# Performance work log

Hardware: AMD Instinct MI355X
Metric: run time of the kernel (lower is better)

The kernel has to match this reference:

```python
import jax, jax.numpy as jnp
import numpy as np

B, S, D, H, A = 2, 2048, 1024, 16, 64
INIT_STD = 0.02


def setup_inputs() -> dict:
    key = jax.random.key(0)
    ks = jax.random.split(key, 5)
    return {
        "residual": jax.random.normal(ks[0], (B, S, D), dtype=jnp.float32),
        "Wq": jax.random.normal(ks[1], (H, D, A), dtype=jnp.float32) * INIT_STD,
        "Wk": jax.random.normal(ks[2], (H, D, A), dtype=jnp.float32) * INIT_STD,
        "Wv": jax.random.normal(ks[3], (H, D, A), dtype=jnp.float32) * INIT_STD,
        "Wo": jax.random.normal(ks[4], (H, A, D), dtype=jnp.float32) * INIT_STD,
        "bq": jnp.zeros((H, A), dtype=jnp.float32),
        "bk": jnp.zeros((H, A), dtype=jnp.float32),
        "bv": jnp.zeros((H, A), dtype=jnp.float32),
        "bo": jnp.zeros((D,), dtype=jnp.float32),
    }


def reference(residual, Wq, Wk, Wv, Wo, bq, bk, bv, bo):
    # residual: [B,S,D]; W{q,k,v}: [H,D,A]; Wo: [H,A,D]
    q = jnp.einsum("bsd,hda->bhsa", residual, Wq) + bq[None, :, None, :]
    k = jnp.einsum("bsd,hda->bhsa", residual, Wk) + bk[None, :, None, :]
    v = jnp.einsum("bsd,hda->bhsa", residual, Wv) + bv[None, :, None, :]
    scale = 1.0 / jnp.sqrt(jnp.float32(q.shape[-1]))
    scores = jnp.einsum("bhsa,bhta->bhst", q, k) * scale  # [B,H,S,S]
    s = scores.shape[-1]
    causal = jnp.tril(jnp.ones((s, s), dtype=bool))  # True = keep
    # original masked_fill with -100000.0 (not -inf); stay faithful
    masked = jnp.where(causal, scores, jnp.float32(-100000.0))
    pattern = jax.nn.softmax(masked, axis=-1)
    z = jnp.einsum("bhst,bhta->bshа".replace("а", "a"), pattern, v)  # [B,S,H,A]
    out = jnp.einsum("bsha,had->bsd", z, Wo) + bo
    return out
```

## Files before the change

kernel.cpp:

```cpp
#include <hip/hip_runtime.h>
#include <hip/hip_bf16.h>

#define B_ 2
#define S_ 2048
#define D_ 1024
#define H_ 16
#define A_ 64

typedef __attribute__((ext_vector_type(8))) short bf16x8;
typedef __attribute__((ext_vector_type(4))) float f32x4;

#define QSCALE 0.1803368801111204f

__device__ inline short f2bf(float f) {
    union { float f; unsigned u; } x; x.f = f;
    unsigned r = x.u + 0x7fff + ((x.u >> 16) & 1);
    return (short)(r >> 16);
}

__device__ inline float dpp_max16(float x) {
    int v;
    v = __builtin_amdgcn_update_dpp(0, __builtin_bit_cast(int, x), 0xB1, 0xF, 0xF, false);
    x = fmaxf(x, __builtin_bit_cast(float, v));
    v = __builtin_amdgcn_update_dpp(0, __builtin_bit_cast(int, x), 0x4E, 0xF, 0xF, false);
    x = fmaxf(x, __builtin_bit_cast(float, v));
    v = __builtin_amdgcn_update_dpp(0, __builtin_bit_cast(int, x), 0x141, 0xF, 0xF, false);
    x = fmaxf(x, __builtin_bit_cast(float, v));
    v = __builtin_amdgcn_update_dpp(0, __builtin_bit_cast(int, x), 0x140, 0xF, 0xF, false);
    x = fmaxf(x, __builtin_bit_cast(float, v));
    return x;
}
__device__ inline float dpp_sum16(float x) {
    int v;
    v = __builtin_amdgcn_update_dpp(0, __builtin_bit_cast(int, x), 0xB1, 0xF, 0xF, false);
    x += __builtin_bit_cast(float, v);
    v = __builtin_amdgcn_update_dpp(0, __builtin_bit_cast(int, x), 0x4E, 0xF, 0xF, false);
    x += __builtin_bit_cast(float, v);
    v = __builtin_amdgcn_update_dpp(0, __builtin_bit_cast(int, x), 0x141, 0xF, 0xF, false);
    x += __builtin_bit_cast(float, v);
    v = __builtin_amdgcn_update_dpp(0, __builtin_bit_cast(int, x), 0x140, 0xF, 0xF, false);
    x += __builtin_bit_cast(float, v);
    return x;
}

__global__ __launch_bounds__(256) void cast_kernel(const float* __restrict__ x,
                                                   short* __restrict__ y, int n) {
    int i = (blockIdx.x * 256 + threadIdx.x) * 8;
    if (i < n) {
        float4 a = *(const float4*)(x + i);
        float4 b = *(const float4*)(x + i + 4);
        bf16x8 o;
        o[0]=f2bf(a.x); o[1]=f2bf(a.y); o[2]=f2bf(a.z); o[3]=f2bf(a.w);
        o[4]=f2bf(b.x); o[5]=f2bf(b.y); o[6]=f2bf(b.z); o[7]=f2bf(b.w);
        *(bf16x8*)(y + i) = o;
    }
}

__global__ __launch_bounds__(256) void wtrans_kernel(
    const float* __restrict__ Wq, const float* __restrict__ Wk,
    const float* __restrict__ Wv, const float* __restrict__ Wo,
    short* __restrict__ Wt, short* __restrict__ Wot) {
    const int kt = blockIdx.x, yy = blockIdx.y, z = blockIdx.z;
    __shared__ short T[64 * 72];
    const int tid = threadIdx.x;
    const int r = tid >> 2, c0 = (tid & 3) * 16;
    const float* src;
    if (z < 3) {
        const float* W = z == 0 ? Wq : (z == 1 ? Wk : Wv);
        src = &W[yy * (D_ * A_) + (kt * 64 + r) * A_ + c0];
    } else {
        src = &Wo[(kt * 64 + r) * D_ + yy * 64 + c0];
    }
    #pragma unroll
    for (int q = 0; q < 4; q++) {
        float4 f = *(const float4*)(src + q * 4);
        T[r * 72 + c0 + q * 4 + 0] = f2bf(f.x);
        T[r * 72 + c0 + q * 4 + 1] = f2bf(f.y);
        T[r * 72 + c0 + q * 4 + 2] = f2bf(f.z);
        T[r * 72 + c0 + q * 4 + 3] = f2bf(f.w);
    }
    __syncthreads();
    const int a = tid >> 2, kc = (tid & 3) * 16;
    bf16x8 o0, o1;
    #pragma unroll
    for (int j = 0; j < 8; j++) {
        o0[j] = T[(kc + j) * 72 + a];
        o1[j] = T[(kc + 8 + j) * 72 + a];
    }
    const int n_base = (z < 3) ? z * 1024 + yy * 64 : yy * 64;
    short* dst = (z < 3) ? &Wt[(n_base + a) * D_ + kt * 64 + kc]
                         : &Wot[(n_base + a) * D_ + kt * 64 + kc];
    *(bf16x8*)dst = o0;
    *(bf16x8*)(dst + 8) = o1;
}

__global__ __launch_bounds__(256) void qkv_gemm(
    const short* __restrict__ X, const short* __restrict__ Wt,
    const float* __restrict__ bq, const float* __restrict__ bk, const float* __restrict__ bv,
    short* __restrict__ Qb, short* __restrict__ Kb, short* __restrict__ Vt) {
    const int mt = blockIdx.x, nt = blockIdx.y;
    const int m0 = mt * 128, n0 = nt * 128;
    const int sel = n0 >> 10;
    __shared__ short Xl[2][128 * 40], Wl[2][128 * 40];
    const int tid = threadIdx.x, wv = tid >> 6, lane = tid & 63, quad = lane >> 4, l16 = lane & 15;
    const int grow = tid >> 1, gk = (tid & 1) * 16;
    f32x4 acc[4][4] = {};
    bf16x8 xr0, xr1, wr0, wr1;
    {
        const short* xs = &X[(m0 + grow) * D_ + gk];
        xr0 = *(const bf16x8*)xs; xr1 = *(const bf16x8*)(xs + 8);
        const short* wsp = &Wt[(n0 + grow) * D_ + gk];
        wr0 = *(const bf16x8*)wsp; wr1 = *(const bf16x8*)(wsp + 8);
    }
    const int rm = (wv & 1) * 64, cn = (wv >> 1) * 64;
    for (int i = 0; i < 32; i++) {
        const int bu = i & 1;
        *(bf16x8*)&Xl[bu][grow * 40 + gk]     = xr0;
        *(bf16x8*)&Xl[bu][grow * 40 + gk + 8] = xr1;
        *(bf16x8*)&Wl[bu][grow * 40 + gk]     = wr0;
        *(bf16x8*)&Wl[bu][grow * 40 + gk + 8] = wr1;
        __syncthreads();
        if (i < 31) {
            const int k0 = (i + 1) * 32;
            const short* xs = &X[(m0 + grow) * D_ + k0 + gk];
            xr0 = *(const bf16x8*)xs; xr1 = *(const bf16x8*)(xs + 8);
            const short* wsp = &Wt[(n0 + grow) * D_ + k0 + gk];
            wr0 = *(const bf16x8*)wsp; wr1 = *(const bf16x8*)(wsp + 8);
        }
        bf16x8 af[4];
        #pragma unroll
        for (int rt = 0; rt < 4; rt++)
            af[rt] = *(bf16x8*)&Xl[bu][(rm + rt * 16 + l16) * 40 + quad * 8];
        #pragma unroll
        for (int ct = 0; ct < 4; ct++) {
            bf16x8 bf = *(bf16x8*)&Wl[bu][(cn + ct * 16 + l16) * 40 + quad * 8];
            #pragma unroll
            for (int rt = 0; rt < 4; rt++)
                acc[rt][ct] = __builtin_amdgcn_mfma_f32_16x16x32_bf16(af[rt], bf, acc[rt][ct], 0, 0, 0);
        }
    }
    const int b = m0 >> 11;
    const float* bias = sel == 0 ? bq : (sel == 1 ? bk : bv);
    if (sel < 2) {
        short* dst = sel == 0 ? Qb : Kb;
        const float scale = sel == 0 ? QSCALE : 1.0f;
        #pragma unroll
        for (int ct = 0; ct < 4; ct++) {
            const int n = n0 + cn + ct * 16 + l16;
            const int h = (n >> 6) & 15, a = n & 63;
            const float bi = bias[n & 1023];
            #pragma unroll
            for (int rt = 0; rt < 4; rt++)
                #pragma unroll
                for (int r = 0; r < 4; r++) {
                    const int row = m0 + rm + rt * 16 + quad * 4 + r;
                    const int s = row & (S_ - 1);
                    dst[(((b * H_) + h) * S_ + s) * A_ + a] = f2bf((acc[rt][ct][r] + bi) * scale);
                }
        }
    } else {
        #pragma unroll
        for (int ct = 0; ct < 4; ct++) {
            const int n = n0 + cn + ct * 16 + l16;
            const int h = (n >> 6) & 15, a = n & 63;
            const float bi = bias[n & 1023];
            #pragma unroll
            for (int rt = 0; rt < 4; rt++) {
                short4 pk;
                pk.x = f2bf(acc[rt][ct][0] + bi);
                pk.y = f2bf(acc[rt][ct][1] + bi);
                pk.z = f2bf(acc[rt][ct][2] + bi);
                pk.w = f2bf(acc[rt][ct][3] + bi);
                const int row = m0 + rm + rt * 16 + quad * 4;
                const int s = row & (S_ - 1);
                *(short4*)&Vt[(((b * H_) + h) * A_ + a) * S_ + s] = pk;
            }
        }
    }
}

__global__ __launch_bounds__(512, 4) void flash_kernel(
    const short* __restrict__ Qb, const short* __restrict__ Kb,
    const short* __restrict__ Vt, short* __restrict__ Z) {
    const int p = blockIdx.x, h = blockIdx.y, b = blockIdx.z;
    const int bh = b * H_ + h;
    const int qlo = p, qhi = 31 - p;
    __shared__ short Kl[2][4096], Vl[2][4096];
    __shared__ short Pl[8][1024];
    const int tid = threadIdx.x, wv = tid >> 6, lane = tid & 63, quad = lane >> 4, l16 = lane & 15;
    const int wg = wv & 3;
    const int myqt = (wv < 4) ? qhi : qlo;
    short* Pw = &Pl[wv][0];
    const int pbase = (l16 >> 3) * 128 + quad * 32 + (l16 & 7);

    const int L = tid;
    const int srow = (L >> 7) * 16 + (L & 15);
    const int scol = ((L >> 6) & 1) * 32 + ((L >> 4) & 3) * 8;

    const short* qptr = &Qb[(bh * S_ + myqt * 64 + wg * 16 + l16) * A_ + quad * 8];
    bf16x8 qf[2] = { *(const bf16x8*)qptr, *(const bf16x8*)(qptr + 32) };

    f32x4 O[4] = {};
    float m_i[4], l_i[4];
    #pragma unroll
    for (int r = 0; r < 4; r++) { m_i[r] = -1e30f; l_i[r] = 0.f; }

    bf16x8 kreg = *(const bf16x8*)&Kb[(bh * S_ + srow) * A_ + scol];
    bf16x8 vreg = *(const bf16x8*)&Vt[(bh * A_ + srow) * S_ + scol];

    for (int kt = 0; kt <= qhi; kt++) {
        const int bu = kt & 1;
        *(bf16x8*)&Kl[bu][L * 8] = kreg;
        *(bf16x8*)&Vl[bu][L * 8] = vreg;
        __syncthreads();
        if (kt < qhi) {
            kreg = *(const bf16x8*)&Kb[(bh * S_ + (kt + 1) * 64 + srow) * A_ + scol];
            vreg = *(const bf16x8*)&Vt[(bh * A_ + srow) * S_ + (kt + 1) * 64 + scol];
        }
        if (kt <= myqt) {
            f32x4 sacc[4] = {};
            #pragma unroll
            for (int kk = 0; kk < 2; kk++)
                #pragma unroll
                for (int ct = 0; ct < 4; ct++) {
                    bf16x8 kf = *(bf16x8*)&Kl[bu][((ct * 2 + kk) * 64 + lane) * 8];
                    sacc[ct] = __builtin_amdgcn_mfma_f32_16x16x32_bf16(qf[kk], kf, sacc[ct], 0, 0, 0);
                }
            if (kt == myqt) {
                #pragma unroll
                for (int ct = 0; ct < 4; ct++) {
                    const int cl = ct * 16 + l16;
                    #pragma unroll
                    for (int r = 0; r < 4; r++)
                        if (cl > wg * 16 + quad * 4 + r) sacc[ct][r] = -1e30f;
                }
            }
            #pragma unroll
            for (int r = 0; r < 4; r++) {
                float v = fmaxf(fmaxf(sacc[0][r], sacc[1][r]), fmaxf(sacc[2][r], sacc[3][r]));
                v = dpp_max16(v);
                const float mn = fmaxf(m_i[r], v);
                const float alpha = exp2f(m_i[r] - mn);
                float rs = 0.f;
                #pragma unroll
                for (int ct = 0; ct < 4; ct++) {
                    const float pe = exp2f(sacc[ct][r] - mn);
                    sacc[ct][r] = pe; rs += pe;
                }
                l_i[r] = l_i[r] * alpha + rs;
                m_i[r] = mn;
                #pragma unroll
                for (int ct = 0; ct < 4; ct++) O[ct][r] *= alpha;
            }
            #pragma unroll
            for (int ct = 0; ct < 4; ct++) {
                const int cb = pbase + (ct >> 1) * 512 + (ct & 1) * 256;
                #pragma unroll
                for (int r = 0; r < 4; r++)
                    Pw[cb + r * 8] = f2bf(sacc[ct][r]);
            }
            __builtin_amdgcn_s_waitcnt(0xC07F);
            bf16x8 pa0 = *(bf16x8*)&Pw[lane * 8];
            bf16x8 pa1 = *(bf16x8*)&Pw[(64 + lane) * 8];
            #pragma unroll
            for (int kk = 0; kk < 2; kk++)
                #pragma unroll
                for (int ct = 0; ct < 4; ct++) {
                    bf16x8 vf = *(bf16x8*)&Vl[bu][((ct * 2 + kk) * 64 + lane) * 8];
                    O[ct] = __builtin_amdgcn_mfma_f32_16x16x32_bf16(kk ? pa1 : pa0, vf, O[ct], 0, 0, 0);
                }
        }
    }
    float lsum[4];
    #pragma unroll
    for (int r = 0; r < 4; r++) lsum[r] = dpp_sum16(l_i[r]);
    #pragma unroll
    for (int ct = 0; ct < 4; ct++) {
        const int a = ct * 16 + l16;
        #pragma unroll
        for (int r = 0; r < 4; r++) {
            const int s = myqt * 64 + wg * 16 + quad * 4 + r;
            Z[(b * S_ + s) * (H_ * A_) + h * A_ + a] = f2bf(O[ct][r] / lsum[r]);
        }
    }
}

__global__ __launch_bounds__(256) void proj_gemm(
    const short* __restrict__ Zb, const short* __restrict__ Wot,
    const float* __restrict__ bo, float* __restrict__ out) {
    const int mt = blockIdx.x, nt = blockIdx.y;
    const int m0 = mt * 128, n0 = nt * 64;
    __shared__ short Xl[2][128 * 40], Wl[2][64 * 40];
    const int tid = threadIdx.x, wv = tid >> 6, lane = tid & 63, quad = lane >> 4, l16 = lane & 15;
    const int grow = tid >> 1, gk = (tid & 1) * 16;
    const bool doW = (tid < 128);
    f32x4 acc[4][2] = {};
    bf16x8 xr0, xr1, wr0, wr1;
    {
        const short* xs = &Zb[(m0 + grow) * D_ + gk];
        xr0 = *(const bf16x8*)xs; xr1 = *(const bf16x8*)(xs + 8);
        if (doW) {
            const short* wsp = &Wot[(n0 + grow) * D_ + gk];
            wr0 = *(const bf16x8*)wsp; wr1 = *(const bf16x8*)(wsp + 8);
        }
    }
    const int rm = (wv & 1) * 64, cn = (wv >> 1) * 32;
    for (int i = 0; i < 32; i++) {
        const int bu = i & 1;
        *(bf16x8*)&Xl[bu][grow * 40 + gk]     = xr0;
        *(bf16x8*)&Xl[bu][grow * 40 + gk + 8] = xr1;
        if (doW) {
            *(bf16x8*)&Wl[bu][grow * 40 + gk]     = wr0;
            *(bf16x8*)&Wl[bu][grow * 40 + gk + 8] = wr1;
        }
        __syncthreads();
        if (i < 31) {
            const int k0 = (i + 1) * 32;
            const short* xs = &Zb[(m0 + grow) * D_ + k0 + gk];
            xr0 = *(const bf16x8*)xs; xr1 = *(const bf16x8*)(xs + 8);
            if (doW) {
                const short* wsp = &Wot[(n0 + grow) * D_ + k0 + gk];
                wr0 = *(const bf16x8*)wsp; wr1 = *(const bf16x8*)(wsp + 8);
            }
        }
        bf16x8 af[4];
        #pragma unroll
        for (int rt = 0; rt < 4; rt++)
            af[rt] = *(bf16x8*)&Xl[bu][(rm + rt * 16 + l16) * 40 + quad * 8];
        #pragma unroll
        for (int ct = 0; ct < 2; ct++) {
            bf16x8 bf = *(bf16x8*)&Wl[bu][(cn + ct * 16 + l16) * 40 + quad * 8];
            #pragma unroll
            for (int rt = 0; rt < 4; rt++)
                acc[rt][ct] = __builtin_amdgcn_mfma_f32_16x16x32_bf16(af[rt], bf, acc[rt][ct], 0, 0, 0);
        }
    }
    #pragma unroll
    for (int ct = 0; ct < 2; ct++) {
        const int n = n0 + cn + ct * 16 + l16;
        const float bi = bo[n];
        #pragma unroll
        for (int rt = 0; rt < 4; rt++)
            #pragma unroll
            for (int r = 0; r < 4; r++) {
                const int row = m0 + rm + rt * 16 + quad * 4 + r;
                out[row * D_ + n] = acc[rt][ct][r] + bi;
            }
    }
}

extern "C" void kernel_launch(void* const* d_in, const int* in_sizes, int n_in,
                              void* d_out, int out_size, void* d_ws, size_t ws_size,
                              hipStream_t stream) {
    const float* residual = (const float*)d_in[0];
    const float* Wq = (const float*)d_in[1];
    const float* Wk = (const float*)d_in[2];
    const float* Wv = (const float*)d_in[3];
    const float* Wo = (const float*)d_in[4];
    const float* bq = (const float*)d_in[5];
    const float* bk = (const float*)d_in[6];
    const float* bv = (const float*)d_in[7];
    const float* bo = (const float*)d_in[8];
    float* out = (float*)d_out;

    char* ws = (char*)d_ws;
    const size_t NE = (size_t)B_ * S_ * D_;
    short* Xbf = (short*)(ws);
    short* Wt  = (short*)(ws +  8ull * 1024 * 1024);
    short* Wot = (short*)(ws + 14ull * 1024 * 1024);
    short* Qb  = (short*)(ws + 16ull * 1024 * 1024);
    short* Kb  = (short*)(ws + 24ull * 1024 * 1024);
    short* Vt  = (short*)(ws + 32ull * 1024 * 1024);
    short* Zb  = (short*)(ws + 40ull * 1024 * 1024);

    hipLaunchKernelGGL(cast_kernel, dim3((int)(NE / (256 * 8))), dim3(256), 0, stream,
                       residual, Xbf, (int)NE);
    hipLaunchKernelGGL(wtrans_kernel, dim3(16, 16, 4), dim3(256), 0, stream,
                       Wq, Wk, Wv, Wo, Wt, Wot);
    hipLaunchKernelGGL(qkv_gemm, dim3(32, 24), dim3(256), 0, stream,
                       Xbf, Wt, bq, bk, bv, Qb, Kb, Vt);
    hipLaunchKernelGGL(flash_kernel, dim3(16, H_, B_), dim3(512), 0, stream,
                       Qb, Kb, Vt, Zb);
    hipLaunchKernelGGL(proj_gemm, dim3(32, 16), dim3(256), 0, stream,
                       Zb, Wot, bo, out);
}
```

Baseline: 209.1 us.

## Transpose flash attention MFMA to keep P in registers via permlane swaps

Swaps the MFMA operand order so score tiles come out transposed, with each lane holding one query row. The softmax row max and sum then become per-lane work plus two cross-quad permlane swaps instead of per-row DPP reductions. P is packed to bf16 with v_cvt_pk_bf16_f32 and rearranged with permlane32/16 swaps into the A-operand layout, which removes the LDS round trip and its waitcnt. The output is written as short4 vectors, and the inline asm and permlane builtins tie the kernel to gfx950.

```diff
diff --git a/kernel.cpp b/kernel.cpp
--- a/kernel.cpp
+++ b/kernel.cpp
@@ -9,6 +9,8 @@
 
 typedef __attribute__((ext_vector_type(8))) short bf16x8;
 typedef __attribute__((ext_vector_type(4))) float f32x4;
+typedef __attribute__((ext_vector_type(4))) unsigned int u32x4;
+typedef __attribute__((ext_vector_type(2))) unsigned int u32x2;
 
 #define QSCALE 0.1803368801111204f
 
@@ -18,29 +20,34 @@
     return (short)(r >> 16);
 }
 
-__device__ inline float dpp_max16(float x) {
-    int v;
-    v = __builtin_amdgcn_update_dpp(0, __builtin_bit_cast(int, x), 0xB1, 0xF, 0xF, false);
-    x = fmaxf(x, __builtin_bit_cast(float, v));
-    v = __builtin_amdgcn_update_dpp(0, __builtin_bit_cast(int, x), 0x4E, 0xF, 0xF, false);
-    x = fmaxf(x, __builtin_bit_cast(float, v));
-    v = __builtin_amdgcn_update_dpp(0, __builtin_bit_cast(int, x), 0x141, 0xF, 0xF, false);
-    x = fmaxf(x, __builtin_bit_cast(float, v));
-    v = __builtin_amdgcn_update_dpp(0, __builtin_bit_cast(int, x), 0x140, 0xF, 0xF, false);
-    x = fmaxf(x, __builtin_bit_cast(float, v));
-    return x;
-}
-__device__ inline float dpp_sum16(float x) {
-    int v;
-    v = __builtin_amdgcn_update_dpp(0, __builtin_bit_cast(int, x), 0xB1, 0xF, 0xF, false);
-    x += __builtin_bit_cast(float, v);
-    v = __builtin_amdgcn_update_dpp(0, __builtin_bit_cast(int, x), 0x4E, 0xF, 0xF, false);
-    x += __builtin_bit_cast(float, v);
-    v = __builtin_amdgcn_update_dpp(0, __builtin_bit_cast(int, x), 0x141, 0xF, 0xF, false);
-    x += __builtin_bit_cast(float, v);
-    v = __builtin_amdgcn_update_dpp(0, __builtin_bit_cast(int, x), 0x140, 0xF, 0xF, false);
-    x += __builtin_bit_cast(float, v);
-    return x;
+__device__ inline unsigned cvt_pk_bf16(float lo, float hi) {
+    unsigned r;
+    asm("v_cvt_pk_bf16_f32 %0, %1, %2" : "=v"(r) : "v"(lo), "v"(hi));
+    return r;
+}
+__device__ inline void pl32swap(unsigned &a, unsigned &b) {
+    u32x2 r = __builtin_amdgcn_permlane32_swap(a, b, false, false);
+    a = r[0]; b = r[1];
+}
+__device__ inline void pl16swap(unsigned &a, unsigned &b) {
+    u32x2 r = __builtin_amdgcn_permlane16_swap(a, b, false, false);
+    a = r[0]; b = r[1];
+}
+__device__ inline float cross_quad_max(float x) {
+    unsigned a = __builtin_bit_cast(unsigned, x), b = a;
+    pl32swap(a, b);
+    float y = fmaxf(__builtin_bit_cast(float, a), __builtin_bit_cast(float, b));
+    unsigned c = __builtin_bit_cast(unsigned, y), d = c;
+    pl16swap(c, d);
+    return fmaxf(__builtin_bit_cast(float, c), __builtin_bit_cast(float, d));
+}
+__device__ inline float cross_quad_sum(float x) {
+    unsigned a = __builtin_bit_cast(unsigned, x), b = a;
+    pl32swap(a, b);
+    float y = __builtin_bit_cast(float, a) + __builtin_bit_cast(float, b);
+    unsigned c = __builtin_bit_cast(unsigned, y), d = c;
+    pl16swap(c, d);
+    return __builtin_bit_cast(float, c) + __builtin_bit_cast(float, d);
 }
 
 __global__ __launch_bounds__(256) void cast_kernel(const float* __restrict__ x,
@@ -186,12 +193,10 @@
     const int bh = b * H_ + h;
     const int qlo = p, qhi = 31 - p;
     __shared__ short Kl[2][4096], Vl[2][4096];
-    __shared__ short Pl[8][1024];
     const int tid = threadIdx.x, wv = tid >> 6, lane = tid & 63, quad = lane >> 4, l16 = lane & 15;
     const int wg = wv & 3;
     const int myqt = (wv < 4) ? qhi : qlo;
-    short* Pw = &Pl[wv][0];
-    const int pbase = (l16 >> 3) * 128 + quad * 32 + (l16 & 7);
+    const int qpos = wg * 16 + l16;
 
     const int L = tid;
     const int srow = (L >> 7) * 16 + (L & 15);
@@ -201,9 +206,7 @@
     bf16x8 qf[2] = { *(const bf16x8*)qptr, *(const bf16x8*)(qptr + 32) };
 
     f32x4 O[4] = {};
-    float m_i[4], l_i[4];
-    #pragma unroll
-    for (int r = 0; r < 4; r++) { m_i[r] = -1e30f; l_i[r] = 0.f; }
+    float m_i = -1e30f, l_i = 0.f;
 
     bf16x8 kreg = *(const bf16x8*)&Kb[(bh * S_ + srow) * A_ + scol];
     bf16x8 vreg = *(const bf16x8*)&Vt[(bh * A_ + srow) * S_ + scol];
@@ -224,64 +227,68 @@
                 #pragma unroll
                 for (int ct = 0; ct < 4; ct++) {
                     bf16x8 kf = *(bf16x8*)&Kl[bu][((ct * 2 + kk) * 64 + lane) * 8];
-                    sacc[ct] = __builtin_amdgcn_mfma_f32_16x16x32_bf16(qf[kk], kf, sacc[ct], 0, 0, 0);
+                    sacc[ct] = __builtin_amdgcn_mfma_f32_16x16x32_bf16(kf, qf[kk], sacc[ct], 0, 0, 0);
                 }
             if (kt == myqt) {
                 #pragma unroll
-                for (int ct = 0; ct < 4; ct++) {
-                    const int cl = ct * 16 + l16;
+                for (int ct = 0; ct < 4; ct++)
                     #pragma unroll
                     for (int r = 0; r < 4; r++)
-                        if (cl > wg * 16 + quad * 4 + r) sacc[ct][r] = -1e30f;
-                }
-            }
-            #pragma unroll
-            for (int r = 0; r < 4; r++) {
-                float v = fmaxf(fmaxf(sacc[0][r], sacc[1][r]), fmaxf(sacc[2][r], sacc[3][r]));
-                v = dpp_max16(v);
-                const float mn = fmaxf(m_i[r], v);
-                const float alpha = exp2f(m_i[r] - mn);
-                float rs = 0.f;
-                #pragma unroll
-                for (int ct = 0; ct < 4; ct++) {
-                    const float pe = exp2f(sacc[ct][r] - mn);
-                    sacc[ct][r] = pe; rs += pe;
-                }
-                l_i[r] = l_i[r] * alpha + rs;
-                m_i[r] = mn;
-                #pragma unroll
-                for (int ct = 0; ct < 4; ct++) O[ct][r] *= alpha;
-            }
-            #pragma unroll
-            for (int ct = 0; ct < 4; ct++) {
-                const int cb = pbase + (ct >> 1) * 512 + (ct & 1) * 256;
+                        if (ct * 16 + quad * 4 + r > qpos) sacc[ct][r] = -1e30f;
+            }
+            f32x4 t4;
+            #pragma unroll
+            for (int r = 0; r < 4; r++)
+                t4[r] = fmaxf(fmaxf(sacc[0][r], sacc[1][r]), fmaxf(sacc[2][r], sacc[3][r]));
+            float vmax = fmaxf(fmaxf(t4[0], t4[1]), fmaxf(t4[2], t4[3]));
+            vmax = cross_quad_max(vmax);
+            const float mn = fmaxf(m_i, vmax);
+            const float alpha = exp2f(m_i - mn);
+            m_i = mn;
+            #pragma unroll
+            for (int ct = 0; ct < 4; ct++)
                 #pragma unroll
                 for (int r = 0; r < 4; r++)
-                    Pw[cb + r * 8] = f2bf(sacc[ct][r]);
-            }
-            __builtin_amdgcn_s_waitcnt(0xC07F);
-            bf16x8 pa0 = *(bf16x8*)&Pw[lane * 8];
-            bf16x8 pa1 = *(bf16x8*)&Pw[(64 + lane) * 8];
-            #pragma unroll
-            for (int kk = 0; kk < 2; kk++)
+                    sacc[ct][r] = exp2f(sacc[ct][r] - mn);
+            f32x4 ps;
+            #pragma unroll
+            for (int r = 0; r < 4; r++)
+                ps[r] = (sacc[0][r] + sacc[1][r]) + (sacc[2][r] + sacc[3][r]);
+            float rs = (ps[0] + ps[1]) + (ps[2] + ps[3]);
+            rs = cross_quad_sum(rs);
+            l_i = l_i * alpha + rs;
+            #pragma unroll
+            for (int ct = 0; ct < 4; ct++) O[ct] *= alpha;
+            #pragma unroll
+            for (int kk = 0; kk < 2; kk++) {
+                unsigned A0 = cvt_pk_bf16(sacc[2 * kk][0], sacc[2 * kk][1]);
+                unsigned A1 = cvt_pk_bf16(sacc[2 * kk][2], sacc[2 * kk][3]);
+                unsigned B0 = cvt_pk_bf16(sacc[2 * kk + 1][0], sacc[2 * kk + 1][1]);
+                unsigned B1 = cvt_pk_bf16(sacc[2 * kk + 1][2], sacc[2 * kk + 1][3]);
+                pl32swap(A0, B0);
+                pl16swap(A0, B0);
+                pl32swap(A1, B1);
+                pl16swap(A1, B1);
+                u32x4 wu; wu[0] = A0; wu[1] = A1; wu[2] = B0; wu[3] = B1;
+                bf16x8 pb = __builtin_bit_cast(bf16x8, wu);
                 #pragma unroll
                 for (int ct = 0; ct < 4; ct++) {
                     bf16x8 vf = *(bf16x8*)&Vl[bu][((ct * 2 + kk) * 64 + lane) * 8];
-                    O[ct] = __builtin_amdgcn_mfma_f32_16x16x32_bf16(kk ? pa1 : pa0, vf, O[ct], 0, 0, 0);
+                    O[ct] = __builtin_amdgcn_mfma_f32_16x16x32_bf16(vf, pb, O[ct], 0, 0, 0);
                 }
-        }
-    }
-    float lsum[4];
-    #pragma unroll
-    for (int r = 0; r < 4; r++) lsum[r] = dpp_sum16(l_i[r]);
+            }
+        }
+    }
+    const float inv = 1.0f / l_i;
+    const int s = myqt * 64 + wg * 16 + l16;
     #pragma unroll
     for (int ct = 0; ct < 4; ct++) {
-        const int a = ct * 16 + l16;
-        #pragma unroll
-        for (int r = 0; r < 4; r++) {
-            const int s = myqt * 64 + wg * 16 + quad * 4 + r;
-            Z[(b * S_ + s) * (H_ * A_) + h * A_ + a] = f2bf(O[ct][r] / lsum[r]);
-        }
+        short4 o4;
+        o4.x = f2bf(O[ct][0] * inv);
+        o4.y = f2bf(O[ct][1] * inv);
+        o4.z = f2bf(O[ct][2] * inv);
+        o4.w = f2bf(O[ct][3] * inv);
+        *(short4*)&Z[(b * S_ + s) * (H_ * A_) + h * A_ + ct * 16 + quad * 4] = o4;
     }
 }
 
```

New measurement: 199.1 us. -4.8%, faster.
